# Kernel optimization log

Hardware: AMD Instinct MI355X
Metric: run time of the kernel (lower is better)

The kernel has to match this reference:

```python
import jax, jax.numpy as jnp
import numpy as np

SEQ_LEN, BATCH, EMB, HID, VOCAB, NLAYERS = 128, 64, 512, 512, 10000, 2


def setup_inputs() -> dict:
    key = jax.random.key(0)
    ks = jax.random.split(key, 8)
    s = 0.1
    return {
        "inputs": jax.random.randint(ks[0], (SEQ_LEN, BATCH), 0, VOCAB, dtype=jnp.int32),
        "hidden": jnp.zeros((NLAYERS, BATCH, HID), jnp.float32),
        "emb_table": jax.random.normal(ks[1], (VOCAB, EMB), jnp.float32) * s,
        "W_x": jax.random.normal(ks[2], (NLAYERS, HID, 3 * HID), jnp.float32) * s,
        "U_h": jax.random.normal(ks[3], (NLAYERS, HID, 2 * HID), jnp.float32) * s,
        "U_ht": jax.random.normal(ks[4], (NLAYERS, HID, HID), jnp.float32) * s,
        "b_rzh": jnp.zeros((NLAYERS, 3 * HID), jnp.float32),
        "fc_W": jax.random.normal(ks[5], (NLAYERS, HID, HID), jnp.float32) * s,
        "fc_b": jnp.zeros((NLAYERS, HID), jnp.float32),
        "dec_W": jax.random.normal(ks[6], (VOCAB, HID), jnp.float32) * s,
        "dec_b": jnp.zeros((VOCAB,), jnp.float32),
    }


def reference(inputs, hidden, emb_table, W_x, U_h, U_ht, b_rzh, fc_W, fc_b, dec_W, dec_b):
    # embeddings: (T, B, E)
    embs = emb_table[inputs]

    def step(h_prev, x_t):
        inp = x_t
        hs = []
        for l in range(NLAYERS):
            gates_x = inp @ W_x[l] + b_rzh[l]          # (B, 3H)
            gates_h = h_prev[l] @ U_h[l]               # (B, 2H)
            Wrx, Wzx, Whx = jnp.split(gates_x, 3, axis=1)
            Urh, Uzh = jnp.split(gates_h, 2, axis=1)
            r = jax.nn.sigmoid(Wrx + Urh)
            z = jax.nn.sigmoid(Wzx + Uzh)
            h_tilde = jnp.tanh(Whx + (r * h_prev[l]) @ U_ht[l])
            h = (1.0 - z) * h_prev[l] + z * h_tilde
            hs.append(h)
            inp = h @ fc_W[l].T + fc_b[l]              # non-recurrent fc (dropout=identity)
        logits_t = inp @ dec_W.T + dec_b               # (B, V)
        return jnp.stack(hs), logits_t

    h_final, logits = jax.lax.scan(step, hidden, embs)
    return logits, h_final
```

## Files before the change

### kernel.cpp

```cpp
#include <hip/hip_runtime.h>
#include <hip/hip_bf16.h>
#include <math.h>

#define TT 128
#define BB 64
#define HH 512
#define VV 10000
#define TBm (TT*BB)
#define H3 (3*HH)
#define H2 (2*HH)

typedef short bf16x8 __attribute__((ext_vector_type(8)));
typedef float f32x4 __attribute__((ext_vector_type(4)));
typedef __hip_bfloat16 bf16;


__global__ void k_init_h(const float* __restrict__ hid, float* __restrict__ h0, float* __restrict__ h1) {
    int g = blockIdx.x * 256 + threadIdx.x;
    if (g < BB*HH) h0[g] = hid[g];
    else           h1[g - BB*HH] = hid[g];
}

__global__ void k_hfinal(const float* __restrict__ h0, const float* __restrict__ h1, float* __restrict__ outp) {
    int g = blockIdx.x * 256 + threadIdx.x;
    outp[g] = (g < BB*HH) ? h0[g] : h1[g - BB*HH];
}

__global__ void k_gather(const int* __restrict__ tok, const float* __restrict__ emb, float* __restrict__ X) {
    size_t g = (size_t)blockIdx.x * 256 + threadIdx.x;
    int row = (int)(g >> 9);
    int e   = (int)(g & 511);
    X[g] = emb[(size_t)tok[row] * HH + e];
}

__global__ void k_cvt(const float* __restrict__ in, bf16* __restrict__ out, int n) {
    int g = blockIdx.x * 256 + threadIdx.x;
    if (g < n) out[g] = __float2bfloat16(in[g]);
}

__global__ void k_a01(const float* __restrict__ fcW0, const float* __restrict__ Wx1, float* __restrict__ A01) {
    int j = blockIdx.x * 256 + threadIdx.x;
    int k = blockIdx.y;
    float a = 0.f;
    for (int i = 0; i < HH; i++) a = fmaf(fcW0[(size_t)i * HH + k], Wx1[(size_t)i * H3 + j], a);
    A01[(size_t)k * H3 + j] = a;
}

__global__ void k_b01(const float* __restrict__ fcb0, const float* __restrict__ Wx1,
                      const float* __restrict__ brzh1, float* __restrict__ b01) {
    int j = blockIdx.x * 256 + threadIdx.x;
    float a = brzh1[j];
    for (int i = 0; i < HH; i++) a = fmaf(fcb0[i], Wx1[(size_t)i * H3 + j], a);
    b01[j] = a;
}

__global__ __launch_bounds__(256) void gemm_f32(const float* __restrict__ A,
                                                const float* __restrict__ W,
                                                const float* __restrict__ bias,
                                                float* __restrict__ C,
                                                int M, int N, int K) {
    __shared__ float As[16][68];
    __shared__ float Ws[16][68];
    const int tid = threadIdx.x;
    const int tx = tid & 15, ty = tid >> 4;
    const int m0 = blockIdx.y * 64, n0 = blockIdx.x * 64;
    float acc[4][4];
    for (int i = 0; i < 4; i++) for (int j = 0; j < 4; j++) acc[i][j] = 0.f;

    const int ar = tid >> 2, ac4 = (tid & 3) * 4;
    const int wk = tid >> 4, wc = (tid & 15) * 4;

    for (int kk = 0; kk < K; kk += 16) {
        float4 av = *(const float4*)&A[(size_t)(m0 + ar) * K + kk + ac4];
        As[ac4 + 0][ar] = av.x; As[ac4 + 1][ar] = av.y;
        As[ac4 + 2][ar] = av.z; As[ac4 + 3][ar] = av.w;
        *(float4*)&Ws[wk][wc] = *(const float4*)&W[(size_t)(kk + wk) * N + n0 + wc];
        __syncthreads();
        #pragma unroll
        for (int k = 0; k < 16; k++) {
            float4 a = *(const float4*)&As[k][ty * 4];
            float4 w = *(const float4*)&Ws[k][tx * 4];
            acc[0][0] = fmaf(a.x, w.x, acc[0][0]); acc[0][1] = fmaf(a.x, w.y, acc[0][1]);
            acc[0][2] = fmaf(a.x, w.z, acc[0][2]); acc[0][3] = fmaf(a.x, w.w, acc[0][3]);
            acc[1][0] = fmaf(a.y, w.x, acc[1][0]); acc[1][1] = fmaf(a.y, w.y, acc[1][1]);
            acc[1][2] = fmaf(a.y, w.z, acc[1][2]); acc[1][3] = fmaf(a.y, w.w, acc[1][3]);
            acc[2][0] = fmaf(a.z, w.x, acc[2][0]); acc[2][1] = fmaf(a.z, w.y, acc[2][1]);
            acc[2][2] = fmaf(a.z, w.z, acc[2][2]); acc[2][3] = fmaf(a.z, w.w, acc[2][3]);
            acc[3][0] = fmaf(a.w, w.x, acc[3][0]); acc[3][1] = fmaf(a.w, w.y, acc[3][1]);
            acc[3][2] = fmaf(a.w, w.z, acc[3][2]); acc[3][3] = fmaf(a.w, w.w, acc[3][3]);
        }
        __syncthreads();
    }
    for (int i = 0; i < 4; i++) {
        size_t row = (size_t)(m0 + ty * 4 + i) * N;
        for (int j = 0; j < 4; j++) {
            int col = n0 + tx * 4 + j;
            C[row + col] = acc[i][j] + bias[col];
        }
    }
}

template<bool OUT_BF16>
__global__ __launch_bounds__(256) void gemm_bt(const ushort* __restrict__ A,
                                               const ushort* __restrict__ B,
                                               const float* __restrict__ bias,
                                               void* __restrict__ Cout,
                                               int M, int N, int K) {
    __shared__ ushort As[128 * 40];
    __shared__ ushort Bs[128 * 40];
    const int tid  = threadIdx.x;
    const int m0   = blockIdx.y * 128;
    const int n0   = blockIdx.x * 128;
    const int wave = tid >> 6, lane = tid & 63;
    const int wm   = (wave >> 1) * 64, wn = (wave & 1) * 64;
    const int l16  = lane & 15, quad = lane >> 4;

    f32x4 acc[4][4];
    {
        f32x4 zz = {0.f, 0.f, 0.f, 0.f};
        for (int i = 0; i < 4; i++) for (int j = 0; j < 4; j++) acc[i][j] = zz;
    }

    for (int kk = 0; kk < K; kk += 32) {
        for (int q = tid; q < 512; q += 256) {
            int r = q >> 2, c = (q & 3) * 8;
            *(bf16x8*)&As[r * 40 + c] = *(const bf16x8*)&A[(size_t)(m0 + r) * K + kk + c];
        }
        for (int q = tid; q < 512; q += 256) {
            int r = q >> 2, c = (q & 3) * 8;
            bf16x8 v; for (int i = 0; i < 8; i++) v[i] = 0;
            if (n0 + r < N) v = *(const bf16x8*)&B[(size_t)(n0 + r) * K + kk + c];
            *(bf16x8*)&Bs[r * 40 + c] = v;
        }
        __syncthreads();
        bf16x8 af[4], bg[4];
        for (int mi = 0; mi < 4; mi++) af[mi] = *(const bf16x8*)&As[(wm + mi * 16 + l16) * 40 + quad * 8];
        for (int ni = 0; ni < 4; ni++) bg[ni] = *(const bf16x8*)&Bs[(wn + ni * 16 + l16) * 40 + quad * 8];
        for (int mi = 0; mi < 4; mi++)
            for (int ni = 0; ni < 4; ni++)
                acc[mi][ni] = __builtin_amdgcn_mfma_f32_16x16x32_bf16(af[mi], bg[ni], acc[mi][ni], 0, 0, 0);
        __syncthreads();
    }

    for (int mi = 0; mi < 4; mi++)
        for (int ni = 0; ni < 4; ni++) {
            int col = n0 + wn + ni * 16 + l16;
            if (col < N) {
                float bs = bias[col];
                for (int r = 0; r < 4; r++) {
                    int row = m0 + wm + mi * 16 + quad * 4 + r;
                    float o = acc[mi][ni][r] + bs;
                    if (OUT_BF16) ((bf16*)Cout)[(size_t)row * N + col] = __float2bfloat16(o);
                    else          ((float*)Cout)[(size_t)row * N + col] = o;
                }
            }
        }
}

__global__ void k_s1(const float* __restrict__ h0, const float* __restrict__ h1,
                     const float* __restrict__ Uh0, const float* __restrict__ Uh1,
                     const float* __restrict__ GX0_t,
                     float* __restrict__ rh0, float* __restrict__ z0, float* __restrict__ gh1) {
    __shared__ float hs[HH];
    int g = blockIdx.x * 256 + threadIdx.x;
    if (g < BB * HH) {
        int b = g >> 9, j = g & (HH - 1);
        const float* hv = h0 + (b << 9);
        for (int k = threadIdx.x; k < HH; k += 256) hs[k] = hv[k];
        __syncthreads();
        float dr = 0.f, dz = 0.f;
        #pragma unroll 8
        for (int k = 0; k < HH; k++) {
            float h = hs[k];
            dr = fmaf(h, Uh0[k * H2 + j], dr);
            dz = fmaf(h, Uh0[k * H2 + HH + j], dz);
        }
        float r = 1.f / (1.f + expf(-(dr + GX0_t[b * H3 + j])));
        float z = 1.f / (1.f + expf(-(dz + GX0_t[b * H3 + HH + j])));
        rh0[g] = r * hs[j];
        z0[g]  = z;
    } else {
        int g2 = g - BB * HH;
        int b = g2 >> 10, j = g2 & (H2 - 1);
        const float* hv = h1 + (b << 9);
        for (int k = threadIdx.x; k < HH; k += 256) hs[k] = hv[k];
        __syncthreads();
        float d = 0.f;
        #pragma unroll 8
        for (int k = 0; k < HH; k++) d = fmaf(hs[k], Uh1[k * H2 + j], d);
        gh1[g2] = d;
    }
}

__global__ void k_s2(float* __restrict__ h0, const float* __restrict__ rh0,
                     const float* __restrict__ z0, const float* __restrict__ Uht0,
                     const float* __restrict__ GX0_t) {
    __shared__ float hs[HH];
    int g = blockIdx.x * 256 + threadIdx.x;
    int b = g >> 9, j = g & (HH - 1);
    const float* rv = rh0 + (b << 9);
    for (int k = threadIdx.x; k < HH; k += 256) hs[k] = rv[k];
    __syncthreads();
    float t0 = 0.f;
    #pragma unroll 8
    for (int k = 0; k < HH; k++) t0 = fmaf(hs[k], Uht0[k * HH + j], t0);
    float ht = tanhf(GX0_t[b * H3 + 2 * HH + j] + t0);
    float z = z0[g];
    float h = h0[g];
    h0[g] = (1.f - z) * h + z * ht;
}

__global__ void k_s3(const float* __restrict__ h0, const float* __restrict__ h1,
                     const float* __restrict__ A01, const float* __restrict__ b01,
                     const float* __restrict__ gh1,
                     float* __restrict__ rh1, float* __restrict__ z1s, float* __restrict__ gxh1) {
    __shared__ float hs[HH];
    int g = blockIdx.x * 256 + threadIdx.x;
    int b = g >> 9, j = g & (HH - 1);
    const float* hv = h0 + (b << 9);
    for (int k = threadIdx.x; k < HH; k += 256) hs[k] = hv[k];
    __syncthreads();
    float ar = 0.f, az = 0.f, ah = 0.f;
    #pragma unroll 4
    for (int k = 0; k < HH; k++) {
        float h = hs[k];
        const float* Ar = A01 + (size_t)k * H3 + j;
        ar = fmaf(h, Ar[0], ar);
        az = fmaf(h, Ar[HH], az);
        ah = fmaf(h, Ar[2 * HH], ah);
    }
    ar += b01[j]; az += b01[HH + j]; ah += b01[2 * HH + j];
    float r = 1.f / (1.f + expf(-(ar + gh1[b * H2 + j])));
    float z = 1.f / (1.f + expf(-(az + gh1[b * H2 + HH + j])));
    rh1[g]  = r * h1[g];
    z1s[g]  = z;
    gxh1[g] = ah;
}

__global__ void k_s4(float* __restrict__ h1, const float* __restrict__ rh1,
                     const float* __restrict__ z1s, const float* __restrict__ gxh1,
                     const float* __restrict__ Uht1, bf16* __restrict__ H1bf_t) {
    __shared__ float hs[HH];
    int g = blockIdx.x * 256 + threadIdx.x;
    int b = g >> 9, j = g & (HH - 1);
    const float* rv = rh1 + (b << 9);
    for (int k = threadIdx.x; k < HH; k += 256) hs[k] = rv[k];
    __syncthreads();
    float t1 = 0.f;
    #pragma unroll 8
    for (int k = 0; k < HH; k++) t1 = fmaf(hs[k], Uht1[k * HH + j], t1);
    float ht = tanhf(gxh1[g] + t1);
    float z = z1s[g];
    float h = h1[g];
    float hn = (1.f - z) * h + z * ht;
    h1[g] = hn;
    H1bf_t[g] = __float2bfloat16(hn);
}

extern "C" void kernel_launch(void* const* d_in, const int* in_sizes, int n_in,
                              void* d_out, int out_size, void* d_ws, size_t ws_size,
                              hipStream_t stream) {
    const int*   tok  = (const int*)d_in[0];
    const float* hid  = (const float*)d_in[1];
    const float* emb  = (const float*)d_in[2];
    const float* W_x  = (const float*)d_in[3];
    const float* U_h  = (const float*)d_in[4];
    const float* U_ht = (const float*)d_in[5];
    const float* brzh = (const float*)d_in[6];
    const float* fcW  = (const float*)d_in[7];
    const float* fcb  = (const float*)d_in[8];
    const float* decW = (const float*)d_in[9];
    const float* decb = (const float*)d_in[10];
    float* out = (float*)d_out;

    char* p = (char*)d_ws;
    auto carve = [&](size_t bytes) { char* r = p; p += (bytes + 255) & ~(size_t)255; return r; };
    float* GX0   = (float*)carve((size_t)TBm * H3 * 4);
    float* Xf    = (float*)carve((size_t)TBm * HH * 4);
    bf16* fcW1b  = (bf16*)carve((size_t)HH * HH * 2);
    bf16* decWb  = (bf16*)carve((size_t)VV * HH * 2);
    bf16* H1bf   = (bf16*)carve((size_t)TBm * HH * 2);
    float* A01   = (float*)carve((size_t)HH * H3 * 4);
    float* b01   = (float*)carve((size_t)H3 * 4);
    float* h0    = (float*)carve((size_t)BB * HH * 4);
    float* h1    = (float*)carve((size_t)BB * HH * 4);
    float* gh1   = (float*)carve((size_t)BB * H2 * 4);
    float* rh0   = (float*)carve((size_t)BB * HH * 4);
    float* z0    = (float*)carve((size_t)BB * HH * 4);
    float* rh1   = (float*)carve((size_t)BB * HH * 4);
    float* z1s   = (float*)carve((size_t)BB * HH * 4);
    float* gxh1  = (float*)carve((size_t)BB * HH * 4);
    bf16* Inp2b  = (bf16*)Xf;

    const float* Uh0  = U_h;
    const float* Uh1  = U_h + (size_t)HH * H2;
    const float* Uht0 = U_ht;
    const float* Uht1 = U_ht + (size_t)HH * HH;
    const float* Wx1  = W_x + (size_t)HH * H3;

    k_init_h<<<256, 256, 0, stream>>>(hid, h0, h1);
    k_gather<<<(TBm * HH) / 256, 256, 0, stream>>>(tok, emb, Xf);
    k_cvt<<<(HH * HH + 255) / 256, 256, 0, stream>>>(fcW + (size_t)HH * HH, fcW1b, HH * HH);
    k_cvt<<<(VV * HH + 255) / 256, 256, 0, stream>>>(decW, decWb, VV * HH);
    k_a01<<<dim3(6, 512), 256, 0, stream>>>(fcW, Wx1, A01);
    k_b01<<<6, 256, 0, stream>>>(fcb, Wx1, brzh + H3, b01);
    gemm_f32<<<dim3(H3 / 64, TBm / 64), 256, 0, stream>>>(Xf, W_x, brzh, GX0, TBm, H3, HH);

    for (int t = 0; t < TT; t++) {
        const float* GX0_t = GX0 + (size_t)t * BB * H3;
        k_s1<<<384, 256, 0, stream>>>(h0, h1, Uh0, Uh1, GX0_t, rh0, z0, gh1);
        k_s2<<<128, 256, 0, stream>>>(h0, rh0, z0, Uht0, GX0_t);
        k_s3<<<128, 256, 0, stream>>>(h0, h1, A01, b01, gh1, rh1, z1s, gxh1);
        k_s4<<<128, 256, 0, stream>>>(h1, rh1, z1s, gxh1, Uht1, H1bf + (size_t)t * BB * HH);
    }

    gemm_bt<true><<<dim3(HH / 128, TBm / 128), 256, 0, stream>>>(
        (const ushort*)H1bf, (const ushort*)fcW1b, fcb + HH, Inp2b, TBm, HH, HH);
    gemm_bt<false><<<dim3((VV + 127) / 128, TBm / 128), 256, 0, stream>>>(
        (const ushort*)Inp2b, (const ushort*)decWb, decb, out, TBm, VV, HH);

    k_hfinal<<<256, 256, 0, stream>>>(h0, h1, out + (size_t)TBm * VV);
}
```

Measured before the change: 16.89 ms.

## Replace per-timestep kernel launches with one persistent cooperative recurrence kernel

Replaces the 512 small per-step launches with a single cooperative kernel that loops over all timesteps and separates phases with grid-wide syncs. Each phase is now a split-K tiled GEMM staged through shared memory (64x64 tiles, 4x4 register blocking), writing partial sums that the next phase reduces while applying the gate nonlinearities. It also uses faster __expf-based sigmoid and tanh and ping-pong buffers for the hidden state. This removes launch overhead and improves weight reuse, at the cost of grid.sync latency, more partial-sum traffic and slightly different rounding.

```diff
diff --git a/kernel.cpp b/kernel.cpp
--- a/kernel.cpp
+++ b/kernel.cpp
@@ -1,6 +1,9 @@
 #include <hip/hip_runtime.h>
 #include <hip/hip_bf16.h>
+#include <hip/hip_cooperative_groups.h>
 #include <math.h>
+
+namespace cg = cooperative_groups;
 
 #define TT 128
 #define BB 64
@@ -19,11 +22,6 @@
     int g = blockIdx.x * 256 + threadIdx.x;
     if (g < BB*HH) h0[g] = hid[g];
     else           h1[g - BB*HH] = hid[g];
-}
-
-__global__ void k_hfinal(const float* __restrict__ h0, const float* __restrict__ h1, float* __restrict__ outp) {
-    int g = blockIdx.x * 256 + threadIdx.x;
-    outp[g] = (g < BB*HH) ? h0[g] : h1[g - BB*HH];
 }
 
 __global__ void k_gather(const int* __restrict__ tok, const float* __restrict__ emb, float* __restrict__ X) {
@@ -157,104 +155,224 @@
         }
 }
 
-__global__ void k_s1(const float* __restrict__ h0, const float* __restrict__ h1,
-                     const float* __restrict__ Uh0, const float* __restrict__ Uh1,
-                     const float* __restrict__ GX0_t,
-                     float* __restrict__ rh0, float* __restrict__ z0, float* __restrict__ gh1) {
-    __shared__ float hs[HH];
-    int g = blockIdx.x * 256 + threadIdx.x;
-    if (g < BB * HH) {
-        int b = g >> 9, j = g & (HH - 1);
-        const float* hv = h0 + (b << 9);
-        for (int k = threadIdx.x; k < HH; k += 256) hs[k] = hv[k];
-        __syncthreads();
-        float dr = 0.f, dz = 0.f;
-        #pragma unroll 8
-        for (int k = 0; k < HH; k++) {
-            float h = hs[k];
-            dr = fmaf(h, Uh0[k * H2 + j], dr);
-            dz = fmaf(h, Uh0[k * H2 + HH + j], dz);
-        }
-        float r = 1.f / (1.f + expf(-(dr + GX0_t[b * H3 + j])));
-        float z = 1.f / (1.f + expf(-(dz + GX0_t[b * H3 + HH + j])));
-        rh0[g] = r * hs[j];
-        z0[g]  = z;
-    } else {
-        int g2 = g - BB * HH;
-        int b = g2 >> 10, j = g2 & (H2 - 1);
-        const float* hv = h1 + (b << 9);
-        for (int k = threadIdx.x; k < HH; k += 256) hs[k] = hv[k];
-        __syncthreads();
-        float d = 0.f;
-        #pragma unroll 8
-        for (int k = 0; k < HH; k++) d = fmaf(hs[k], Uh1[k * H2 + j], d);
-        gh1[g2] = d;
-    }
-}
-
-__global__ void k_s2(float* __restrict__ h0, const float* __restrict__ rh0,
-                     const float* __restrict__ z0, const float* __restrict__ Uht0,
-                     const float* __restrict__ GX0_t) {
-    __shared__ float hs[HH];
-    int g = blockIdx.x * 256 + threadIdx.x;
-    int b = g >> 9, j = g & (HH - 1);
-    const float* rv = rh0 + (b << 9);
-    for (int k = threadIdx.x; k < HH; k += 256) hs[k] = rv[k];
-    __syncthreads();
-    float t0 = 0.f;
+
+__device__ __forceinline__ float sigm_f(float x) { return 1.f / (1.f + __expf(-x)); }
+__device__ __forceinline__ float tanh_f(float x) {
+    float ax = fabsf(x);
+    float e  = __expf(-2.f * ax);
+    float t  = (1.f - e) / (1.f + e);
+    return copysignf(t, x);
+}
+__device__ __forceinline__ float sum8(const float* __restrict__ p) {
+    float4 a = *(const float4*)p;
+    float4 b = *(const float4*)(p + 4);
+    return ((a.x + a.y) + (a.z + a.w)) + ((b.x + b.y) + (b.z + b.w));
+}
+
+__device__ __forceinline__ void stage_w64(float* __restrict__ ws, const float* __restrict__ W,
+                                          int N, int kb, int jb, int tid) {
+    int k = tid >> 2, jq = (tid & 3) << 4;
+    const float4* s = (const float4*)(W + (size_t)(kb + k) * N + jb + jq);
+    float4* d = (float4*)(ws + k * 68 + jq);
+    d[0] = s[0]; d[1] = s[1]; d[2] = s[2]; d[3] = s[3];
+}
+
+__device__ __forceinline__ void stage_a_plain(float* __restrict__ hs, const float* __restrict__ H,
+                                              int kb, int tid) {
+    int b = tid >> 2, ks = (tid & 3) << 4;
+    const float4* s = (const float4*)(H + b * HH + kb + ks);
+    float v[16];
+    *(float4*)&v[0] = s[0]; *(float4*)&v[4] = s[1]; *(float4*)&v[8] = s[2]; *(float4*)&v[12] = s[3];
+    #pragma unroll
+    for (int i = 0; i < 16; i++) hs[(ks + i) * 68 + b] = v[i];
+}
+
+__device__ __forceinline__ void stage_a_rh0(float* __restrict__ hs, const float* __restrict__ prz,
+                                            const float* __restrict__ GX0t, const float* __restrict__ h0r,
+                                            int kb, int tid) {
+    int b = tid >> 2, ks = (tid & 3) << 4;
+    #pragma unroll 4
+    for (int i = 0; i < 16; i++) {
+        int k = kb + ks + i;
+        float d = sum8(prz + ((b << 10) + k) * 8) + GX0t[b * H3 + k];
+        hs[(ks + i) * 68 + b] = sigm_f(d) * h0r[b * HH + k];
+    }
+}
+
+__device__ __forceinline__ void stage_a_h0n(float* __restrict__ hs, const float* __restrict__ prz,
+                                            const float* __restrict__ pht0, const float* __restrict__ GX0t,
+                                            const float* __restrict__ h0r, float* __restrict__ h0w,
+                                            int kb, int tid, bool wr) {
+    int b = tid >> 2, ks = (tid & 3) << 4;
+    #pragma unroll 4
+    for (int i = 0; i < 16; i++) {
+        int k = kb + ks + i;
+        float z  = sigm_f(sum8(prz + ((b << 10) + HH + k) * 8) + GX0t[b * H3 + HH + k]);
+        float ht = tanh_f(sum8(pht0 + ((b << 9) + k) * 8) + GX0t[b * H3 + 2 * HH + k]);
+        float hp = h0r[b * HH + k];
+        float hn = fmaf(z, ht - hp, hp);
+        hs[(ks + i) * 68 + b] = hn;
+        if (wr) h0w[b * HH + k] = hn;
+    }
+}
+
+__device__ __forceinline__ void stage_a_rh1(float* __restrict__ hs, const float* __restrict__ pg1,
+                                            const float* __restrict__ pgh1, const float* __restrict__ b01,
+                                            const float* __restrict__ h1r, int kb, int tid) {
+    int b = tid >> 2, ks = (tid & 3) << 4;
+    #pragma unroll 4
+    for (int i = 0; i < 16; i++) {
+        int k = kb + ks + i;
+        float d = sum8(pg1 + (b * H3 + k) * 8) + sum8(pgh1 + ((b << 10) + k) * 8) + b01[k];
+        hs[(ks + i) * 68 + b] = sigm_f(d) * h1r[b * HH + k];
+    }
+}
+
+__device__ __forceinline__ void stage_a_h1n(float* __restrict__ hs, const float* __restrict__ pg1,
+                                            const float* __restrict__ pgh1, const float* __restrict__ pht1,
+                                            const float* __restrict__ b01, const float* __restrict__ h1r,
+                                            float* __restrict__ h1w, bf16* __restrict__ Hb,
+                                            int kb, int tid, bool wr) {
+    int b = tid >> 2, ks = (tid & 3) << 4;
+    #pragma unroll 4
+    for (int i = 0; i < 16; i++) {
+        int k = kb + ks + i;
+        float z  = sigm_f(sum8(pg1 + (b * H3 + HH + k) * 8) + sum8(pgh1 + ((b << 10) + HH + k) * 8) + b01[HH + k]);
+        float ht = tanh_f(sum8(pht1 + ((b << 9) + k) * 8) + sum8(pg1 + (b * H3 + 2 * HH + k) * 8) + b01[2 * HH + k]);
+        float hp = h1r[b * HH + k];
+        float hn = fmaf(z, ht - hp, hp);
+        if (hs) hs[(ks + i) * 68 + b] = hn;
+        if (wr) { h1w[b * HH + k] = hn; Hb[b * HH + k] = __float2bfloat16(hn); }
+    }
+}
+
+__device__ __forceinline__ void gemm_store(const float* __restrict__ hs, const float* __restrict__ ws,
+                                           float* __restrict__ P, int N, int kc, int jb, int tid) {
+    const int tx = tid & 15, ty = tid >> 4;
+    float acc[4][4];
+    #pragma unroll
+    for (int i = 0; i < 4; i++)
+        #pragma unroll
+        for (int j = 0; j < 4; j++) acc[i][j] = 0.f;
     #pragma unroll 8
-    for (int k = 0; k < HH; k++) t0 = fmaf(hs[k], Uht0[k * HH + j], t0);
-    float ht = tanhf(GX0_t[b * H3 + 2 * HH + j] + t0);
-    float z = z0[g];
-    float h = h0[g];
-    h0[g] = (1.f - z) * h + z * ht;
-}
-
-__global__ void k_s3(const float* __restrict__ h0, const float* __restrict__ h1,
-                     const float* __restrict__ A01, const float* __restrict__ b01,
-                     const float* __restrict__ gh1,
-                     float* __restrict__ rh1, float* __restrict__ z1s, float* __restrict__ gxh1) {
-    __shared__ float hs[HH];
-    int g = blockIdx.x * 256 + threadIdx.x;
-    int b = g >> 9, j = g & (HH - 1);
-    const float* hv = h0 + (b << 9);
-    for (int k = threadIdx.x; k < HH; k += 256) hs[k] = hv[k];
-    __syncthreads();
-    float ar = 0.f, az = 0.f, ah = 0.f;
-    #pragma unroll 4
-    for (int k = 0; k < HH; k++) {
-        float h = hs[k];
-        const float* Ar = A01 + (size_t)k * H3 + j;
-        ar = fmaf(h, Ar[0], ar);
-        az = fmaf(h, Ar[HH], az);
-        ah = fmaf(h, Ar[2 * HH], ah);
-    }
-    ar += b01[j]; az += b01[HH + j]; ah += b01[2 * HH + j];
-    float r = 1.f / (1.f + expf(-(ar + gh1[b * H2 + j])));
-    float z = 1.f / (1.f + expf(-(az + gh1[b * H2 + HH + j])));
-    rh1[g]  = r * h1[g];
-    z1s[g]  = z;
-    gxh1[g] = ah;
-}
-
-__global__ void k_s4(float* __restrict__ h1, const float* __restrict__ rh1,
-                     const float* __restrict__ z1s, const float* __restrict__ gxh1,
-                     const float* __restrict__ Uht1, bf16* __restrict__ H1bf_t) {
-    __shared__ float hs[HH];
-    int g = blockIdx.x * 256 + threadIdx.x;
-    int b = g >> 9, j = g & (HH - 1);
-    const float* rv = rh1 + (b << 9);
-    for (int k = threadIdx.x; k < HH; k += 256) hs[k] = rv[k];
-    __syncthreads();
-    float t1 = 0.f;
-    #pragma unroll 8
-    for (int k = 0; k < HH; k++) t1 = fmaf(hs[k], Uht1[k * HH + j], t1);
-    float ht = tanhf(gxh1[g] + t1);
-    float z = z1s[g];
-    float h = h1[g];
-    float hn = (1.f - z) * h + z * ht;
-    h1[g] = hn;
-    H1bf_t[g] = __float2bfloat16(hn);
+    for (int k = 0; k < 64; k++) {
+        float4 a = *(const float4*)(hs + k * 68 + ty * 4);
+        float4 w = *(const float4*)(ws + k * 68 + tx * 4);
+        acc[0][0] = fmaf(a.x, w.x, acc[0][0]); acc[0][1] = fmaf(a.x, w.y, acc[0][1]);
+        acc[0][2] = fmaf(a.x, w.z, acc[0][2]); acc[0][3] = fmaf(a.x, w.w, acc[0][3]);
+        acc[1][0] = fmaf(a.y, w.x, acc[1][0]); acc[1][1] = fmaf(a.y, w.y, acc[1][1]);
+        acc[1][2] = fmaf(a.y, w.z, acc[1][2]); acc[1][3] = fmaf(a.y, w.w, acc[1][3]);
+        acc[2][0] = fmaf(a.z, w.x, acc[2][0]); acc[2][1] = fmaf(a.z, w.y, acc[2][1]);
+        acc[2][2] = fmaf(a.z, w.z, acc[2][2]); acc[2][3] = fmaf(a.z, w.w, acc[2][3]);
+        acc[3][0] = fmaf(a.w, w.x, acc[3][0]); acc[3][1] = fmaf(a.w, w.y, acc[3][1]);
+        acc[3][2] = fmaf(a.w, w.z, acc[3][2]); acc[3][3] = fmaf(a.w, w.w, acc[3][3]);
+    }
+    #pragma unroll
+    for (int i = 0; i < 4; i++) {
+        int b = ty * 4 + i;
+        #pragma unroll
+        for (int j = 0; j < 4; j++) {
+            int col = jb + tx * 4 + j;
+            P[((size_t)(b * N + col) << 3) + kc] = acc[i][j];
+        }
+    }
+}
+
+struct RecArgs {
+    const float *GX0, *Uh0, *Uh1, *Uht0, *Uht1, *A01, *b01;
+    float *h0A, *h0B, *h1A, *h1B;
+    float *prz, *pgh1A, *pgh1B, *pht0, *pg1, *pht1;
+    bf16 *H1bf;
+    float *hfin;
+};
+
+__global__ __launch_bounds__(256) void k_rec(RecArgs a) {
+    cg::grid_group grid = cg::this_grid();
+    __shared__ float hs[64 * 68];
+    __shared__ float ws[64 * 68];
+    const int tid = threadIdx.x;
+    const int bid = blockIdx.x;
+
+    for (int t = 0; t < TT; t++) {
+        const float* GX0t = a.GX0 + (size_t)t * BB * H3;
+        float* h0r   = (t & 1) ? a.h0B : a.h0A;
+        float* h0w   = (t & 1) ? a.h0A : a.h0B;
+        float* h1rS1 = ((t + 1) & 1) ? a.h1B : a.h1A;
+        float* h1wS1 = (t & 1) ? a.h1B : a.h1A;
+        float* h1rS4 = h1wS1;
+        float* pgh1w = (t & 1) ? a.pgh1B : a.pgh1A;
+        float* pgh1r = (t & 1) ? a.pgh1A : a.pgh1B;
+
+        for (int c = bid; c < 256; c += gridDim.x) {
+            int g = c >> 7, kc = (c >> 4) & 7, jc = c & 15;
+            int kb = kc << 6, jb = jc << 6;
+            if (g == 0) {
+                stage_a_plain(hs, h0r, kb, tid);
+                stage_w64(ws, a.Uh0, H2, kb, jb, tid);
+                __syncthreads();
+                gemm_store(hs, ws, a.prz, H2, kc, jb, tid);
+            } else {
+                if (t == 0) stage_a_plain(hs, a.h1A, kb, tid);
+                else stage_a_h1n(hs, a.pg1, pgh1r, a.pht1, a.b01, h1rS1, h1wS1,
+                                 a.H1bf + (size_t)(t - 1) * BB * HH, kb, tid, jc == 0);
+                stage_w64(ws, a.Uh1, H2, kb, jb, tid);
+                __syncthreads();
+                gemm_store(hs, ws, pgh1w, H2, kc, jb, tid);
+            }
+            __syncthreads();
+        }
+        grid.sync();
+
+        for (int c = bid; c < 64; c += gridDim.x) {
+            int kc = c >> 3, jc = c & 7;
+            int kb = kc << 6, jb = jc << 6;
+            stage_a_rh0(hs, a.prz, GX0t, h0r, kb, tid);
+            stage_w64(ws, a.Uht0, HH, kb, jb, tid);
+            __syncthreads();
+            gemm_store(hs, ws, a.pht0, HH, kc, jb, tid);
+            __syncthreads();
+        }
+        grid.sync();
+
+        for (int c = bid; c < 192; c += gridDim.x) {
+            int kc = c / 24, jc = c % 24;
+            int kb = kc << 6, jb = jc << 6;
+            stage_a_h0n(hs, a.prz, a.pht0, GX0t, h0r, h0w, kb, tid, jc == 0);
+            stage_w64(ws, a.A01, H3, kb, jb, tid);
+            __syncthreads();
+            gemm_store(hs, ws, a.pg1, H3, kc, jb, tid);
+            __syncthreads();
+        }
+        grid.sync();
+
+        for (int c = bid; c < 64; c += gridDim.x) {
+            int kc = c >> 3, jc = c & 7;
+            int kb = kc << 6, jb = jc << 6;
+            stage_a_rh1(hs, a.pg1, pgh1w, a.b01, h1rS4, kb, tid);
+            stage_w64(ws, a.Uht1, HH, kb, jb, tid);
+            __syncthreads();
+            gemm_store(hs, ws, a.pht1, HH, kc, jb, tid);
+            __syncthreads();
+        }
+        grid.sync();
+    }
+
+    {
+        const float* pgh1r = a.pgh1B;
+        const float* h1r   = a.h1B;
+        for (int c = bid; c < 16; c += gridDim.x) {
+            int kb = (c & 7) << 6;
+            if (c < 8) {
+                stage_a_h1n(nullptr, a.pg1, pgh1r, a.pht1, a.b01, h1r,
+                            a.hfin + BB * HH, a.H1bf + (size_t)127 * BB * HH, kb, tid, true);
+            } else {
+                int b = tid >> 2, ks = (tid & 3) << 4;
+                const float4* s = (const float4*)(a.h0A + b * HH + kb + ks);
+                float4* d = (float4*)(a.hfin + b * HH + kb + ks);
+                d[0] = s[0]; d[1] = s[1]; d[2] = s[2]; d[3] = s[3];
+            }
+        }
+    }
 }
 
 extern "C" void kernel_launch(void* const* d_in, const int* in_sizes, int n_in,
@@ -282,14 +400,17 @@
     bf16* H1bf   = (bf16*)carve((size_t)TBm * HH * 2);
     float* A01   = (float*)carve((size_t)HH * H3 * 4);
     float* b01   = (float*)carve((size_t)H3 * 4);
-    float* h0    = (float*)carve((size_t)BB * HH * 4);
-    float* h1    = (float*)carve((size_t)BB * HH * 4);
-    float* gh1   = (float*)carve((size_t)BB * H2 * 4);
-    float* rh0   = (float*)carve((size_t)BB * HH * 4);
-    float* z0    = (float*)carve((size_t)BB * HH * 4);
-    float* rh1   = (float*)carve((size_t)BB * HH * 4);
-    float* z1s   = (float*)carve((size_t)BB * HH * 4);
-    float* gxh1  = (float*)carve((size_t)BB * HH * 4);
+    float* h0A   = (float*)carve((size_t)BB * HH * 4);
+    float* h0B   = (float*)carve((size_t)BB * HH * 4);
+    float* h1A   = (float*)carve((size_t)BB * HH * 4);
+    float* h1B   = (float*)carve((size_t)BB * HH * 4);
+
+    float* prz   = Xf;
+    float* pgh1A = Xf + 1 * 524288;
+    float* pgh1B = Xf + 2 * 524288;
+    float* pht0  = Xf + 3 * 524288;
+    float* pg1   = Xf + 3 * 524288 + 262144;
+    float* pht1  = pg1 + 786432;
     bf16* Inp2b  = (bf16*)Xf;
 
     const float* Uh0  = U_h;
@@ -298,7 +419,7 @@
     const float* Uht1 = U_ht + (size_t)HH * HH;
     const float* Wx1  = W_x + (size_t)HH * H3;
 
-    k_init_h<<<256, 256, 0, stream>>>(hid, h0, h1);
+    k_init_h<<<256, 256, 0, stream>>>(hid, h0A, h1A);
     k_gather<<<(TBm * HH) / 256, 256, 0, stream>>>(tok, emb, Xf);
     k_cvt<<<(HH * HH + 255) / 256, 256, 0, stream>>>(fcW + (size_t)HH * HH, fcW1b, HH * HH);
     k_cvt<<<(VV * HH + 255) / 256, 256, 0, stream>>>(decW, decWb, VV * HH);
@@ -306,18 +427,18 @@
     k_b01<<<6, 256, 0, stream>>>(fcb, Wx1, brzh + H3, b01);
     gemm_f32<<<dim3(H3 / 64, TBm / 64), 256, 0, stream>>>(Xf, W_x, brzh, GX0, TBm, H3, HH);
 
-    for (int t = 0; t < TT; t++) {
-        const float* GX0_t = GX0 + (size_t)t * BB * H3;
-        k_s1<<<384, 256, 0, stream>>>(h0, h1, Uh0, Uh1, GX0_t, rh0, z0, gh1);
-        k_s2<<<128, 256, 0, stream>>>(h0, rh0, z0, Uht0, GX0_t);
-        k_s3<<<128, 256, 0, stream>>>(h0, h1, A01, b01, gh1, rh1, z1s, gxh1);
-        k_s4<<<128, 256, 0, stream>>>(h1, rh1, z1s, gxh1, Uht1, H1bf + (size_t)t * BB * HH);
-    }
+    RecArgs ra;
+    ra.GX0 = GX0; ra.Uh0 = Uh0; ra.Uh1 = Uh1; ra.Uht0 = Uht0; ra.Uht1 = Uht1;
+    ra.A01 = A01; ra.b01 = b01;
+    ra.h0A = h0A; ra.h0B = h0B; ra.h1A = h1A; ra.h1B = h1B;
+    ra.prz = prz; ra.pgh1A = pgh1A; ra.pgh1B = pgh1B;
+    ra.pht0 = pht0; ra.pg1 = pg1; ra.pht1 = pht1;
+    ra.H1bf = H1bf; ra.hfin = out + (size_t)TBm * VV;
+    void* kargs[] = { &ra };
+    hipLaunchCooperativeKernel(k_rec, dim3(256), dim3(256), kargs, 0, stream);
 
     gemm_bt<true><<<dim3(HH / 128, TBm / 128), 256, 0, stream>>>(
         (const ushort*)H1bf, (const ushort*)fcW1b, fcb + HH, Inp2b, TBm, HH, HH);
     gemm_bt<false><<<dim3((VV + 127) / 128, TBm / 128), 256, 0, stream>>>(
         (const ushort*)Inp2b, (const ushort*)decWb, decb, out, TBm, VV, HH);
-
-    k_hfinal<<<256, 256, 0, stream>>>(h0, h1, out + (size_t)TBm * VV);
-}
+}
```

After: 28.22 ms. +67.1%, slower.
